# Kernel optimization log

Measured on AMD Instinct MI355X. Metric: run time of the kernel, lower is better.

Reference implementation:

```python
import jax, jax.numpy as jnp
import numpy as np

N_HEADS = 16

def setup_inputs() -> dict:
    key = jax.random.key(0)
    ks = jax.random.split(key, 7)
    B, S, D = 2, 2048, 1024
    sc = 1.0 / np.sqrt(D)
    return {
        "x": jax.random.normal(ks[0], (B, S, D), dtype=jnp.float32),
        "Wq": jax.random.normal(ks[1], (D, D), dtype=jnp.float32) * sc,
        "bq": jax.random.normal(ks[2], (D,), dtype=jnp.float32) * 0.02,
        "Wk": jax.random.normal(ks[3], (D, D), dtype=jnp.float32) * sc,
        "bk": jax.random.normal(ks[4], (D,), dtype=jnp.float32) * 0.02,
        "Wv": jax.random.normal(ks[5], (D, D), dtype=jnp.float32) * sc,
        "bv": jax.random.normal(ks[6], (D,), dtype=jnp.float32) * 0.02,
    }

def reference(x, Wq, bq, Wk, bk, Wv, bv):
    B, S, D = x.shape
    H = N_HEADS
    W = D // H  # head width
    # QKV projections (torch Linear: x @ W^T + b); here weights stored as [D_in, D_out]
    q = x @ Wq + bq
    k = x @ Wk + bk
    v = x @ Wv + bv
    # split last dim into heads -> [B, H, S, W]
    q = q.reshape(B, S, H, W).transpose(0, 2, 1, 3)
    k = k.reshape(B, S, H, W).transpose(0, 2, 1, 3)
    v = v.reshape(B, S, H, W).transpose(0, 2, 1, 3)
    # scaled dot-product attention; full [B,H,S,S] scores as in original
    scores = jnp.einsum("bhqw,bhkw->bhqk", q, k) / jnp.sqrt(jnp.asarray(W, x.dtype))
    probs = jax.nn.softmax(scores, axis=-1)  # dropout is identity in eval mode
    h = jnp.einsum("bhqk,bhkw->bhqw", probs, v)
    # merge heads -> [B, S, D]
    return h.transpose(0, 2, 1, 3).reshape(B, S, D)
```

## Files before the change

### kernel.cpp

```cpp
#include <hip/hip_runtime.h>

typedef _Float16 H16;
typedef _Float16 half8 __attribute__((ext_vector_type(8)));
typedef _Float16 half4 __attribute__((ext_vector_type(4)));
typedef float f32x4 __attribute__((ext_vector_type(4)));

constexpr int Bb = 2, S = 2048, D = 1024, NH = 16, HW = 64;
constexpr int M = Bb * S;

constexpr size_t XH_OFF = 0;
constexpr size_t WT_OFF = XH_OFF + (size_t)M * D * 2;
constexpr size_t Q_OFF  = WT_OFF + 3ull * D * D * 2;
constexpr size_t K_OFF  = Q_OFF + (size_t)M * D * 2;
constexpr size_t VT_OFF = K_OFF + (size_t)M * D * 2;

#define GLOAD_LDS16(g, l)                                        \
  __builtin_amdgcn_global_load_lds(                              \
      (const __attribute__((address_space(1))) void*)(g),        \
      (__attribute__((address_space(3))) void*)(l), 16, 0, 0)

__global__ __launch_bounds__(256) void prep(const float* __restrict__ x,
                                            H16* __restrict__ xh,
                                            const float* __restrict__ w0,
                                            const float* __restrict__ w1,
                                            const float* __restrict__ w2,
                                            H16* __restrict__ wt) {
  __shared__ H16 tile[64][65];
  const int z = blockIdx.z;
  const int t = threadIdx.x;
  if (z == 0) {
    const int bid = blockIdx.y * 16 + blockIdx.x;
#pragma unroll
    for (int r = 0; r < 8; ++r) {
      size_t i = ((size_t)(bid * 8 + r) * 256 + t) * 8;
      float4 a = *(const float4*)(x + i);
      float4 b = *(const float4*)(x + i + 4);
      half8 h = {(H16)a.x, (H16)a.y, (H16)a.z, (H16)a.w,
                 (H16)b.x, (H16)b.y, (H16)b.z, (H16)b.w};
      *(half8*)(xh + i) = h;
    }
  } else {
    const float* w = z == 1 ? w0 : z == 2 ? w1 : w2;
    H16* out = wt + (size_t)(z - 1) * D * D;
    int c = t & 63, r4 = t >> 6;
    int bx = blockIdx.x * 64, by = blockIdx.y * 64;
#pragma unroll 4
    for (int it = 0; it < 16; ++it) {
      int row = it * 4 + r4;
      tile[c][row] = (H16)w[(size_t)(by + row) * D + bx + c];
    }
    __syncthreads();
#pragma unroll 4
    for (int it = 0; it < 16; ++it) {
      int row = it * 4 + r4;
      out[(size_t)(bx + row) * D + by + c] = tile[row][c];
    }
  }
}

__global__ __launch_bounds__(256) void qkv_gemm(
    const H16* __restrict__ xh, const H16* __restrict__ wt,
    const float* __restrict__ bq, const float* __restrict__ bk,
    const float* __restrict__ bv, H16* __restrict__ qo, H16* __restrict__ ko,
    H16* __restrict__ vto) {
  __shared__ __align__(16) H16 As[128 * 32];
  __shared__ __align__(16) H16 Bs[128 * 32];
  const int z = blockIdx.z;
  const H16* w = wt + (size_t)z * D * D;
  const float* bias = z == 0 ? bq : z == 1 ? bk : bv;
  const int bm = blockIdx.y * 128, bn = blockIdx.x * 128;
  const int t = threadIdx.x;
  const int wave = t >> 6, lane = t & 63;
  const int g = lane >> 4, c = lane & 15;
  const int wm = (wave >> 1) * 64, wn = (wave & 1) * 64;

  f32x4 acc[4][4] = {};

  for (int kk = 0; kk < D; kk += 32) {
#pragma unroll
    for (int rnd = 0; rnd < 2; ++rnd) {
      int cid = rnd * 256 + t;
      int row = cid >> 2, k0 = (cid & 3) * 8;
      GLOAD_LDS16(&xh[(size_t)(bm + row) * D + kk + k0], &As[cid * 8]);
      GLOAD_LDS16(&w[(size_t)(bn + row) * D + kk + k0], &Bs[cid * 8]);
    }
    __syncthreads();
    half8 af[4], bf[4];
#pragma unroll
    for (int i = 0; i < 4; ++i) {
      af[i] = *(const half8*)&As[(wm + i * 16 + c) * 32 + g * 8];
      bf[i] = *(const half8*)&Bs[(wn + i * 16 + c) * 32 + g * 8];
    }
#pragma unroll
    for (int i = 0; i < 4; ++i)
#pragma unroll
      for (int j = 0; j < 4; ++j)
        acc[i][j] =
            __builtin_amdgcn_mfma_f32_16x16x32_f16(af[i], bf[j], acc[i][j], 0, 0, 0);
    __syncthreads();
  }

#pragma unroll
  for (int i = 0; i < 4; ++i) {
#pragma unroll
    for (int j = 0; j < 4; ++j) {
      int coln = bn + wn + j * 16 + c;
      float bse = bias[coln];
      int h = coln >> 6, wcol = coln & 63;
      if (z == 2) {
        int row0 = bm + wm + i * 16 + g * 4;
        int bbx = row0 >> 11, s0 = row0 & (S - 1);
        half4 v4 = {(H16)(acc[i][j][0] + bse), (H16)(acc[i][j][1] + bse),
                    (H16)(acc[i][j][2] + bse), (H16)(acc[i][j][3] + bse)};
        *(half4*)&vto[((size_t)(bbx * NH + h) * HW + wcol) * S + s0] = v4;
      } else {
#pragma unroll
        for (int r = 0; r < 4; ++r) {
          int row = bm + wm + i * 16 + g * 4 + r;
          float val = acc[i][j][r] + bse;
          int bbx = row >> 11, s = row & (S - 1);
          size_t bh = (size_t)(bbx * NH + h);
          if (z == 0)
            qo[(bh * S + s) * HW + wcol] = (H16)val;
          else
            ko[(bh * S + s) * HW + wcol] = (H16)val;
        }
      }
    }
  }
}

__global__ __launch_bounds__(512, 4) void attn(const H16* __restrict__ q,
                                               const H16* __restrict__ k,
                                               const H16* __restrict__ vt,
                                               float* __restrict__ out) {
  constexpr int NIT = S / 128;
  __shared__ __align__(16) H16 Ks[2][64 * 64];
  __shared__ __align__(16) H16 Vs[2][64 * 64];
  __shared__ __align__(16) H16 pl[8][32 * 64];
  __shared__ float lx[4][2][16];

  const int id = blockIdx.x;
  const int xcd = id & 7, slot = id >> 3;
  const int bh = xcd * 4 + (slot >> 4);
  const int qt = slot & 15;

  const int t = threadIdx.x, wave = t >> 6, lane = t & 63;
  const int kg = wave >> 2, w4 = wave & 3;
  const int g = lane >> 4, c = lane & 15;
  const int q0 = qt * 128 + w4 * 32;
  const H16* qp = q + ((size_t)bh * S + q0) * HW;
  const H16* kp = k + ((size_t)bh * S + kg * (S / 2)) * HW;
  const H16* vp = vt + (size_t)bh * HW * S + kg * (S / 2);

  const int tt = t & 255;
  const int r0 = tt >> 3, k8 = tt & 7;
  const int r1 = r0 + 32;
  const int wsw0 = r0 * 64 + ((k8 ^ (r0 & 7)) * 8);
  const int wsw1 = r1 * 64 + ((k8 ^ (r1 & 7)) * 8);
  H16* ksb = Ks[kg];
  H16* vsb = Vs[kg];

  const H16 scq = (H16)(0.125f * 1.44269504088896f);
  half8 qb[2][2];
#pragma unroll
  for (int qg = 0; qg < 2; ++qg) {
    qb[qg][0] = *(const half8*)&qp[(qg * 16 + c) * HW + g * 8];
    qb[qg][1] = *(const half8*)&qp[(qg * 16 + c) * HW + 32 + g * 8];
#pragma unroll
    for (int e = 0; e < 8; ++e) {
      qb[qg][0][e] *= scq;
      qb[qg][1][e] *= scq;
    }
  }

  f32x4 o[4][2] = {};
  float l[2] = {0.f, 0.f};
  H16* myp = pl[wave];

  const int sw0 = (g ^ (c & 7)) * 8;
  const int sw1 = ((4 + g) ^ (c & 7)) * 8;
  int pwc[4];
#pragma unroll
  for (int kt = 0; kt < 4; ++kt)
    pwc[kt] = (((kt * 2 + (g >> 1)) ^ (c & 7)) * 8) + (g & 1) * 4;

  {
    half8 ka = *(const half8*)&kp[(size_t)r0 * HW + k8 * 8];
    half8 kb = *(const half8*)&kp[(size_t)r1 * HW + k8 * 8];
    half8 va = *(const half8*)&vp[(size_t)r0 * S + k8 * 8];
    half8 vb = *(const half8*)&vp[(size_t)r1 * S + k8 * 8];
    *(half8*)&ksb[wsw0] = ka;
    *(half8*)&ksb[wsw1] = kb;
    *(half8*)&vsb[wsw0] = va;
    *(half8*)&vsb[wsw1] = vb;
  }

  for (int it = 0; it < NIT; ++it) {
    __syncthreads();

    half8 nka, nkb, nva, nvb;
    if (it + 1 < NIT) {
      const int nck = (it + 1) * 64;
      nka = *(const half8*)&kp[(size_t)(nck + r0) * HW + k8 * 8];
      nkb = *(const half8*)&kp[(size_t)(nck + r1) * HW + k8 * 8];
      nva = *(const half8*)&vp[(size_t)r0 * S + nck + k8 * 8];
      nvb = *(const half8*)&vp[(size_t)r1 * S + nck + k8 * 8];
    }

    f32x4 st[4][2];
#pragma unroll
    for (int kt = 0; kt < 4; ++kt) {
      const H16* kr = &ksb[(kt * 16 + c) * 64];
      half8 ka0 = *(const half8*)&kr[sw0];
      half8 ka1 = *(const half8*)&kr[sw1];
#pragma unroll
      for (int qg = 0; qg < 2; ++qg) {
        f32x4 z = {};
        st[kt][qg] =
            __builtin_amdgcn_mfma_f32_16x16x32_f16(ka0, qb[qg][0], z, 0, 0, 0);
        st[kt][qg] = __builtin_amdgcn_mfma_f32_16x16x32_f16(ka1, qb[qg][1],
                                                            st[kt][qg], 0, 0, 0);
      }
    }

    half8 pb[2][2];
#pragma unroll
    for (int qg = 0; qg < 2; ++qg) {
#pragma unroll
      for (int kt = 0; kt < 4; ++kt) {
        float p0 = __builtin_amdgcn_exp2f(st[kt][qg][0]);
        float p1 = __builtin_amdgcn_exp2f(st[kt][qg][1]);
        float p2 = __builtin_amdgcn_exp2f(st[kt][qg][2]);
        float p3 = __builtin_amdgcn_exp2f(st[kt][qg][3]);
        l[qg] += (p0 + p1) + (p2 + p3);
        half4 pk = {(H16)p0, (H16)p1, (H16)p2, (H16)p3};
        *(half4*)&myp[(qg * 16 + c) * 64 + pwc[kt]] = pk;
      }
      pb[qg][0] = *(const half8*)&myp[(qg * 16 + c) * 64 + sw0];
      pb[qg][1] = *(const half8*)&myp[(qg * 16 + c) * 64 + sw1];
    }

#pragma unroll
    for (int wt = 0; wt < 4; ++wt) {
      const H16* vr = &vsb[(wt * 16 + c) * 64];
      half8 va0 = *(const half8*)&vr[sw0];
      half8 va1 = *(const half8*)&vr[sw1];
#pragma unroll
      for (int qg = 0; qg < 2; ++qg) {
        o[wt][qg] = __builtin_amdgcn_mfma_f32_16x16x32_f16(va0, pb[qg][0],
                                                           o[wt][qg], 0, 0, 0);
        o[wt][qg] = __builtin_amdgcn_mfma_f32_16x16x32_f16(va1, pb[qg][1],
                                                           o[wt][qg], 0, 0, 0);
      }
    }

    __syncthreads();
    if (it + 1 < NIT) {
      *(half8*)&ksb[wsw0] = nka;
      *(half8*)&ksb[wsw1] = nkb;
      *(half8*)&vsb[wsw0] = nva;
      *(half8*)&vsb[wsw1] = nvb;
    }
  }

#pragma unroll
  for (int qg = 0; qg < 2; ++qg) {
    l[qg] += __shfl_xor(l[qg], 16, 64);
    l[qg] += __shfl_xor(l[qg], 32, 64);
  }

  float* pex = (float*)pl;
  if (kg == 1) {
    float* dst = pex + w4 * 2048;
#pragma unroll
    for (int wt = 0; wt < 4; ++wt)
#pragma unroll
      for (int qg = 0; qg < 2; ++qg)
        *(f32x4*)&dst[(wt * 2 + qg) * 256 + lane * 4] = o[wt][qg];
    if (g == 0) {
      lx[w4][0][c] = l[0];
      lx[w4][1][c] = l[1];
    }
  }
  __syncthreads();
  if (kg == 0) {
    const float* src = pex + w4 * 2048;
    const int bbx = bh >> 4, h = bh & 15;
#pragma unroll
    for (int qg = 0; qg < 2; ++qg) {
      const float inv = 1.0f / (l[qg] + lx[w4][qg][c]);
      float* orow = out + ((size_t)bbx * S + q0 + qg * 16 + c) * D + h * HW;
#pragma unroll
      for (int wt = 0; wt < 4; ++wt) {
        f32x4 po = *(const f32x4*)&src[(wt * 2 + qg) * 256 + lane * 4];
        float4 v4 = {(o[wt][qg][0] + po[0]) * inv, (o[wt][qg][1] + po[1]) * inv,
                     (o[wt][qg][2] + po[2]) * inv, (o[wt][qg][3] + po[3]) * inv};
        *(float4*)&orow[wt * 16 + g * 4] = v4;
      }
    }
  }
}

extern "C" void kernel_launch(void* const* d_in, const int* in_sizes, int n_in,
                              void* d_out, int out_size, void* d_ws,
                              size_t ws_size, hipStream_t stream) {
  const float* x = (const float*)d_in[0];
  const float* Wq = (const float*)d_in[1];
  const float* bq = (const float*)d_in[2];
  const float* Wk = (const float*)d_in[3];
  const float* bk = (const float*)d_in[4];
  const float* Wv = (const float*)d_in[5];
  const float* bv = (const float*)d_in[6];
  float* out = (float*)d_out;
  char* ws = (char*)d_ws;
  H16* xh = (H16*)(ws + XH_OFF);
  H16* wt = (H16*)(ws + WT_OFF);
  H16* qw = (H16*)(ws + Q_OFF);
  H16* kw = (H16*)(ws + K_OFF);
  H16* vtw = (H16*)(ws + VT_OFF);

  prep<<<dim3(16, 16, 4), 256, 0, stream>>>(x, xh, Wq, Wk, Wv, wt);
  qkv_gemm<<<dim3(8, 32, 3), 256, 0, stream>>>(xh, wt, bq, bk, bv, qw, kw, vtw);
  attn<<<dim3(512), 512, 0, stream>>>(qw, kw, vtw, out);
}
```

Before: 163.4 us.

## Double-buffer attention K/V via direct-to-LDS loads, keep P in registers, widen GEMM K-tile

The attention kernel now stages K and V tiles straight into double-buffered LDS with global_load_lds, dropping the register round-trip and the second barrier per iteration. Keys are permuted at load time so the softmax probabilities can feed the PV MFMA straight from registers, which removes the per-wave P scratch buffer in LDS. The QKV GEMM K-step grows from 32 to 64, halving its barrier count per tile. The price is more LDS for the K/V double buffers and a tile-load address mapping that is harder to verify; the epilogue reuses the K buffer for the cross-group reduction.

```diff
diff --git a/kernel.cpp b/kernel.cpp
--- a/kernel.cpp
+++ b/kernel.cpp
@@ -63,8 +63,8 @@
     const float* __restrict__ bq, const float* __restrict__ bk,
     const float* __restrict__ bv, H16* __restrict__ qo, H16* __restrict__ ko,
     H16* __restrict__ vto) {
-  __shared__ __align__(16) H16 As[128 * 32];
-  __shared__ __align__(16) H16 Bs[128 * 32];
+  __shared__ __align__(16) H16 As[128 * 64];
+  __shared__ __align__(16) H16 Bs[128 * 64];
   const int z = blockIdx.z;
   const H16* w = wt + (size_t)z * D * D;
   const float* bias = z == 0 ? bq : z == 1 ? bk : bv;
@@ -76,27 +76,30 @@
 
   f32x4 acc[4][4] = {};
 
-  for (int kk = 0; kk < D; kk += 32) {
-#pragma unroll
-    for (int rnd = 0; rnd < 2; ++rnd) {
+  for (int kk = 0; kk < D; kk += 64) {
+#pragma unroll
+    for (int rnd = 0; rnd < 4; ++rnd) {
       int cid = rnd * 256 + t;
-      int row = cid >> 2, k0 = (cid & 3) * 8;
+      int row = cid >> 3, k0 = (cid & 7) * 8;
       GLOAD_LDS16(&xh[(size_t)(bm + row) * D + kk + k0], &As[cid * 8]);
       GLOAD_LDS16(&w[(size_t)(bn + row) * D + kk + k0], &Bs[cid * 8]);
     }
     __syncthreads();
-    half8 af[4], bf[4];
-#pragma unroll
-    for (int i = 0; i < 4; ++i) {
-      af[i] = *(const half8*)&As[(wm + i * 16 + c) * 32 + g * 8];
-      bf[i] = *(const half8*)&Bs[(wn + i * 16 + c) * 32 + g * 8];
-    }
-#pragma unroll
-    for (int i = 0; i < 4; ++i)
-#pragma unroll
-      for (int j = 0; j < 4; ++j)
-        acc[i][j] =
-            __builtin_amdgcn_mfma_f32_16x16x32_f16(af[i], bf[j], acc[i][j], 0, 0, 0);
+#pragma unroll
+    for (int kc = 0; kc < 2; ++kc) {
+      half8 af[4], bf[4];
+#pragma unroll
+      for (int i = 0; i < 4; ++i) {
+        af[i] = *(const half8*)&As[(wm + i * 16 + c) * 64 + kc * 32 + g * 8];
+        bf[i] = *(const half8*)&Bs[(wn + i * 16 + c) * 64 + kc * 32 + g * 8];
+      }
+#pragma unroll
+      for (int i = 0; i < 4; ++i)
+#pragma unroll
+        for (int j = 0; j < 4; ++j)
+          acc[i][j] = __builtin_amdgcn_mfma_f32_16x16x32_f16(af[i], bf[j],
+                                                             acc[i][j], 0, 0, 0);
+    }
     __syncthreads();
   }
 
@@ -135,9 +138,8 @@
                                                const H16* __restrict__ vt,
                                                float* __restrict__ out) {
   constexpr int NIT = S / 128;
-  __shared__ __align__(16) H16 Ks[2][64 * 64];
-  __shared__ __align__(16) H16 Vs[2][64 * 64];
-  __shared__ __align__(16) H16 pl[8][32 * 64];
+  __shared__ __align__(16) H16 Ks[2][2][64 * 64];
+  __shared__ __align__(16) H16 Vs[2][2][64 * 64];
   __shared__ float lx[4][2][16];
 
   const int id = blockIdx.x;
@@ -154,12 +156,21 @@
   const H16* vp = vt + (size_t)bh * HW * S + kg * (S / 2);
 
   const int tt = t & 255;
-  const int r0 = tt >> 3, k8 = tt & 7;
-  const int r1 = r0 + 32;
-  const int wsw0 = r0 * 64 + ((k8 ^ (r0 & 7)) * 8);
-  const int wsw1 = r1 * 64 + ((k8 ^ (r1 & 7)) * 8);
-  H16* ksb = Ks[kg];
-  H16* vsb = Vs[kg];
+  const int sq = tt >> 3, sj = tt & 7;
+  const int kkey = ((sq >> 2) & 3) * 8 + ((sq >> 4) & 1) * 4 + (sq & 3);
+  const int scol = (sj ^ (sq & 7)) * 8;
+  const H16* kga = kp + (size_t)kkey * HW + scol;
+  const H16* kgb = kp + (size_t)(32 + kkey) * HW + scol;
+  const H16* vga = vp + (size_t)sq * S + scol;
+  const H16* vgb = vp + (size_t)(sq + 32) * S + scol;
+
+#define STAGE(bufi, nck)                                                  \
+  {                                                                       \
+    GLOAD_LDS16(kga + (size_t)(nck) * HW, &Ks[bufi][kg][tt * 8]);         \
+    GLOAD_LDS16(kgb + (size_t)(nck) * HW, &Ks[bufi][kg][2048 + tt * 8]);  \
+    GLOAD_LDS16(vga + (nck), &Vs[bufi][kg][tt * 8]);                      \
+    GLOAD_LDS16(vgb + (nck), &Vs[bufi][kg][2048 + tt * 8]);               \
+  }
 
   const H16 scq = (H16)(0.125f * 1.44269504088896f);
   half8 qb[2][2];
@@ -176,42 +187,23 @@
 
   f32x4 o[4][2] = {};
   float l[2] = {0.f, 0.f};
-  H16* myp = pl[wave];
 
   const int sw0 = (g ^ (c & 7)) * 8;
   const int sw1 = ((4 + g) ^ (c & 7)) * 8;
-  int pwc[4];
-#pragma unroll
-  for (int kt = 0; kt < 4; ++kt)
-    pwc[kt] = (((kt * 2 + (g >> 1)) ^ (c & 7)) * 8) + (g & 1) * 4;
-
-  {
-    half8 ka = *(const half8*)&kp[(size_t)r0 * HW + k8 * 8];
-    half8 kb = *(const half8*)&kp[(size_t)r1 * HW + k8 * 8];
-    half8 va = *(const half8*)&vp[(size_t)r0 * S + k8 * 8];
-    half8 vb = *(const half8*)&vp[(size_t)r1 * S + k8 * 8];
-    *(half8*)&ksb[wsw0] = ka;
-    *(half8*)&ksb[wsw1] = kb;
-    *(half8*)&vsb[wsw0] = va;
-    *(half8*)&vsb[wsw1] = vb;
-  }
-
+
+  STAGE(0, 0);
+  int buf = 0;
   for (int it = 0; it < NIT; ++it) {
     __syncthreads();
-
-    half8 nka, nkb, nva, nvb;
-    if (it + 1 < NIT) {
-      const int nck = (it + 1) * 64;
-      nka = *(const half8*)&kp[(size_t)(nck + r0) * HW + k8 * 8];
-      nkb = *(const half8*)&kp[(size_t)(nck + r1) * HW + k8 * 8];
-      nva = *(const half8*)&vp[(size_t)r0 * S + nck + k8 * 8];
-      nvb = *(const half8*)&vp[(size_t)r1 * S + nck + k8 * 8];
-    }
+    if (it + 1 < NIT) STAGE(buf ^ 1, (it + 1) * 64);
+
+    const H16* ks = Ks[buf][kg];
+    const H16* vs = Vs[buf][kg];
 
     f32x4 st[4][2];
 #pragma unroll
     for (int kt = 0; kt < 4; ++kt) {
-      const H16* kr = &ksb[(kt * 16 + c) * 64];
+      const H16* kr = &ks[(kt * 16 + c) * 64];
       half8 ka0 = *(const half8*)&kr[sw0];
       half8 ka1 = *(const half8*)&kr[sw1];
 #pragma unroll
@@ -234,16 +226,16 @@
         float p2 = __builtin_amdgcn_exp2f(st[kt][qg][2]);
         float p3 = __builtin_amdgcn_exp2f(st[kt][qg][3]);
         l[qg] += (p0 + p1) + (p2 + p3);
-        half4 pk = {(H16)p0, (H16)p1, (H16)p2, (H16)p3};
-        *(half4*)&myp[(qg * 16 + c) * 64 + pwc[kt]] = pk;
-      }
-      pb[qg][0] = *(const half8*)&myp[(qg * 16 + c) * 64 + sw0];
-      pb[qg][1] = *(const half8*)&myp[(qg * 16 + c) * 64 + sw1];
+        pb[qg][kt >> 1][(kt & 1) * 4 + 0] = (H16)p0;
+        pb[qg][kt >> 1][(kt & 1) * 4 + 1] = (H16)p1;
+        pb[qg][kt >> 1][(kt & 1) * 4 + 2] = (H16)p2;
+        pb[qg][kt >> 1][(kt & 1) * 4 + 3] = (H16)p3;
+      }
     }
 
 #pragma unroll
     for (int wt = 0; wt < 4; ++wt) {
-      const H16* vr = &vsb[(wt * 16 + c) * 64];
+      const H16* vr = &vs[(wt * 16 + c) * 64];
       half8 va0 = *(const half8*)&vr[sw0];
       half8 va1 = *(const half8*)&vr[sw1];
 #pragma unroll
@@ -254,15 +246,9 @@
                                                            o[wt][qg], 0, 0, 0);
       }
     }
-
-    __syncthreads();
-    if (it + 1 < NIT) {
-      *(half8*)&ksb[wsw0] = nka;
-      *(half8*)&ksb[wsw1] = nkb;
-      *(half8*)&vsb[wsw0] = nva;
-      *(half8*)&vsb[wsw1] = nvb;
-    }
-  }
+    buf ^= 1;
+  }
+#undef STAGE
 
 #pragma unroll
   for (int qg = 0; qg < 2; ++qg) {
@@ -270,7 +256,9 @@
     l[qg] += __shfl_xor(l[qg], 32, 64);
   }
 
-  float* pex = (float*)pl;
+  __syncthreads();
+
+  float* pex = (float*)Ks;
   if (kg == 1) {
     float* dst = pex + w4 * 2048;
 #pragma unroll
```

Measured after the change: 180.1 us. +10.2%, slower.
